# Kernel tuning notes

Measured on AMD Instinct MI355X. Metric: run time of the kernel, lower is better.

Reference implementation:

```python
import jax, jax.numpy as jnp
import numpy as np

NEG = -1e30  # finite stand-in for -inf so logsumexp grads stay finite


def ctc_loss_mean(y_true, log_probs_tm, input_length, label_length, blank=0):
    """CTC loss (forward algorithm in log space), mean over batch.

    log_probs_tm: [T, B, C] time-major log-probabilities.
    y_true:       [B, L] dense int labels (blank=0 excluded from real labels).
    """
    T, B, C = log_probs_tm.shape
    L = y_true.shape[1]
    S = 2 * L + 1  # extended label length: blank, l1, blank, l2, ...
    ll = jnp.clip(label_length, 1, L)
    il = jnp.clip(input_length, 1, T)

    # Extended label sequence: blanks at even positions, labels at odd.
    ext = jnp.full((B, S), blank, dtype=jnp.int32).at[:, 1::2].set(y_true.astype(jnp.int32))
    ext_m2 = jnp.concatenate([jnp.full((B, 2), -1, jnp.int32), ext[:, :-2]], axis=1)
    # Skip transition (s-2 -> s) allowed only for label positions with no repeat.
    allow_skip = ((jnp.arange(S) % 2 == 1)[None, :]) & (ext != ext_m2)

    lp0 = jnp.take_along_axis(log_probs_tm[0], ext, axis=1)  # [B, S]
    alpha0 = jnp.full((B, S), NEG, log_probs_tm.dtype)
    alpha0 = alpha0.at[:, 0].set(lp0[:, 0]).at[:, 1].set(lp0[:, 1])

    def step(alpha, xs):
        lp_t, t = xs
        lpe = jnp.take_along_axis(lp_t, ext, axis=1)  # [B, S]
        a1 = jnp.concatenate([jnp.full((B, 1), NEG, alpha.dtype), alpha[:, :-1]], axis=1)
        a2 = jnp.concatenate([jnp.full((B, 2), NEG, alpha.dtype), alpha[:, :-2]], axis=1)
        a2 = jnp.where(allow_skip, a2, NEG)
        new = jax.nn.logsumexp(jnp.stack([alpha, a1, a2]), axis=0) + lpe
        # Freeze alpha once past each example's input_length.
        return jnp.where((t < il)[:, None], new, alpha), None

    alpha, _ = jax.lax.scan(step, alpha0, (log_probs_tm[1:], jnp.arange(1, T)))

    # Loss = -log(alpha[2*ll-1] + alpha[2*ll]) at the final (frozen) time step.
    idx = jnp.stack([2 * ll - 1, 2 * ll], axis=1)  # [B, 2]
    end_vals = jnp.take_along_axis(alpha, idx, axis=1)
    loss = -jax.nn.logsumexp(end_vals, axis=1)
    return jnp.mean(loss)


def setup_inputs() -> dict:
    key = jax.random.key(0)
    kx, kl, ki, kj = jax.random.split(key, 4)
    B, T, C, L = 64, 1024, 128, 256
    # y_pred are probabilities (module applies log), so softmax random logits.
    y_pred = jax.nn.softmax(jax.random.normal(kx, (B, T, C), jnp.float32), axis=-1)
    y_true = jax.random.randint(kl, (B, L), 1, C, jnp.int32)  # blank=0 excluded
    input_length = jax.random.randint(ki, (B,), T // 2, T + 1, jnp.int32)
    label_length = jax.random.randint(kj, (B,), L // 2, L + 1, jnp.int32)
    return {"y_true": y_true, "y_pred": y_pred,
            "input_length": input_length, "label_length": label_length}


def reference(y_true, y_pred, input_length, label_length):
    # Mirror CTCLayer.call: log + transpose to time-major, reshape lengths.
    log_tm = jnp.log(jnp.transpose(y_pred, (1, 0, 2)))  # [T, B, C]
    loss = ctc_loss_mean(y_true, log_tm,
                         input_length.reshape(-1), label_length.reshape(-1),
                         blank=0)
    return log_tm, loss
```

## Files before the change

### kernel.cpp

```cpp
#include <hip/hip_runtime.h>
#include <math.h>

constexpr int B = 64;
constexpr int T = 1024;
constexpr int C = 128;
constexpr int L = 256;
constexpr int S = 2 * L + 1;
constexpr int TRB = 2048;

template <int N> struct IC { static constexpr int value = N; };

__device__ __forceinline__ float shr1(float x) {
#if __has_builtin(__builtin_amdgcn_mov_dpp)
    return __int_as_float(__builtin_amdgcn_mov_dpp(
        __float_as_int(x), 0x138 , 0xf, 0xf, true));
#else
    return __int_as_float(__builtin_amdgcn_update_dpp(
        0, __float_as_int(x), 0x138, 0xf, 0xf, true));
#endif
}

template <int CTRL>
__device__ __forceinline__ float maxdpp(float x) {
#if __has_builtin(__builtin_amdgcn_mov_dpp)
    float t = __int_as_float(__builtin_amdgcn_mov_dpp(
        __float_as_int(x), CTRL, 0xf, 0xf, true));
#else
    float t = __int_as_float(__builtin_amdgcn_update_dpp(
        0, __float_as_int(x), CTRL, 0xf, 0xf, true));
#endif
    return fmaxf(x, t);
}

__device__ __forceinline__ float wave_max_dpp(float x) {
    x = maxdpp<0x111>(x);
    x = maxdpp<0x112>(x);
    x = maxdpp<0x114>(x);
    x = maxdpp<0x118>(x);
    x = maxdpp<0x142>(x);
    x = maxdpp<0x143>(x);
    return __int_as_float(__builtin_amdgcn_readlane(__float_as_int(x), 63));
}

__global__
__attribute__((amdgpu_waves_per_eu(1, 1)))
__launch_bounds__(64)
void ctc_fused(
    const float* __restrict__ yp,
    const int*   __restrict__ yt,
    const int*   __restrict__ il_,
    const int*   __restrict__ ll_,
    float* __restrict__ out_log,
    float* __restrict__ out_loss)
{
    const int lane = threadIdx.x;
    if (blockIdx.x >= B) {
        int id = blockIdx.x - B;
        int bb = id >> 5;
        int ck = id & 31;
        const float4* src = (const float4*)yp + ((size_t)bb * T + ck * 32) * 32;
        float4* o4 = (float4*)out_log;
        #pragma unroll
        for (int k = 0; k < 16; ++k) {
            int o = k * 64 + lane;
            float4 v = src[o];
            int tt = ck * 32 + (o >> 5);
            int c4 = o & 31;
            float4 r;
            r.x = __logf(v.x); r.y = __logf(v.y);
            r.z = __logf(v.z); r.w = __logf(v.w);
            o4[((size_t)tt * B + bb) * 32 + c4] = r;
        }
        return;
    }

    const int b = blockIdx.x;

    __shared__ float afin[S];

    int il = il_[b]; il = min(max(il, 1), T);
    int ll = ll_[b]; ll = min(max(ll, 1), L);
    const float* yb = yp + (size_t)b * T * C;

    int4 y4 = *(const int4*)(yt + b * L + 4 * lane);
    int  pw = yt[b * L + (lane ? 4 * lane - 1 : 0)];

    float skf4 = (lane && (y4.x != pw))   ? 1.f : 0.f;
    float skf5 = (y4.y != y4.x) ? 1.f : 0.f;
    float skf6 = (y4.z != y4.y) ? 1.f : 0.f;
    float skf7 = (y4.w != y4.z) ? 1.f : 0.f;

    const int c0 = y4.x, c1 = y4.y, c2 = y4.z, c3 = y4.w;

    int z0;
    asm volatile("v_mov_b32 %0, 0" : "=v"(z0));

    float gv[3][4][4], gbv[3][4];

    auto fill = [&](auto Qc, int r0) {
        constexpr int Q = decltype(Qc)::value;
        int r = r0 < T - 4 ? r0 : T - 4;
        const float* rb = yb + (size_t)r * C;
        #pragma unroll
        for (int j = 0; j < 4; ++j) {
            gbv[Q][j]   = rb[j * C + z0];
            gv[Q][j][0] = rb[j * C + c0];
            gv[Q][j][1] = rb[j * C + c1];
            gv[Q][j][2] = rb[j * C + c2];
            gv[Q][j][3] = rb[j * C + c3];
        }
    };

    float p00 = yb[0];
    float p0l = yb[c0];

    fill(IC<0>{}, 1);
    fill(IC<1>{}, 5);

    float a[9];
    #pragma unroll
    for (int i = 0; i < 9; ++i) a[i] = 0.f;
    if (lane == 0) { a[0] = p00; a[1] = p0l; }

    int lsi = 0;
    int t0 = 0;

    auto step = [&](float gb, float g0, float g1, float g2, float g3) {
        float hh = shr1(a[7]);
        float n0 = (a[0] + hh)                      * gb;
        float n1 = fmaf(skf4, hh,   a[1] + a[0])    * g0;
        float n2 = (a[2] + a[1])                    * gb;
        float n3 = fmaf(skf5, a[1], a[3] + a[2])    * g1;
        float n4 = (a[4] + a[3])                    * gb;
        float n5 = fmaf(skf6, a[3], a[5] + a[4])    * g2;
        float n6 = (a[6] + a[5])                    * gb;
        float n7 = fmaf(skf7, a[5], a[7] + a[6])    * g3;
        float n8 = (a[8] + a[7])                    * gb;
        a[0] = n0; a[1] = n1; a[2] = n2; a[3] = n3; a[4] = n4;
        a[5] = n5; a[6] = n6; a[7] = n7; a[8] = n8;
    };

    auto group = [&](auto Pc) {
        constexpr int P = decltype(Pc)::value;
        constexpr int F = (P + 2) % 3;
        #pragma unroll
        for (int j = 0; j < 4; ++j)
            step(gbv[P][j], gv[P][j][0], gv[P][j][1], gv[P][j][2], gv[P][j][3]);
        fill(IC<F>{}, t0 + 9);
        __builtin_amdgcn_sched_barrier(0x7);
        t0 += 4;
    };

    auto maxw = [&]() {
        float m0 = fmaxf(fmaxf(a[0], a[1]), a[2]);
        float m1 = fmaxf(fmaxf(a[3], a[4]), a[5]);
        float m2 = fmaxf(fmaxf(a[6], a[7]), a[8]);
        return fmaxf(fmaxf(m0, m1), m2);
    };

    int pinv_bits = 127 << 23;
    int psh = 0;
    auto measure = [&]() {
        float mm = wave_max_dpp(maxw());
        int eb = (__float_as_int(mm) >> 23) & 0xff;
        int sh = 350 - eb;
        sh = sh > 254 ? 254 : (sh < 1 ? 1 : sh);
        pinv_bits = sh << 23;
        psh = sh - 127;
    };
    auto apply = [&]() {
        float inv = __int_as_float(pinv_bits);
        #pragma unroll
        for (int i = 0; i < 9; ++i) a[i] *= inv;
        lsi -= psh;
    };
    auto rescale = [&]() { measure(); apply(); };

    const int full_end = ((il - 1) >> 2) << 2;

    while (t0 + 24 <= full_end) {
        group(IC<0>{});
        apply();
        group(IC<1>{});
        measure();
        group(IC<2>{});
        apply();
        group(IC<0>{});
        measure();
        group(IC<1>{});
        apply();
        group(IC<2>{});
        measure();
    }
    apply();

    if (t0 + 4 <= full_end) { group(IC<0>{}); rescale(); }
    if (t0 + 4 <= full_end) { group(IC<1>{}); rescale(); }
    if (t0 + 4 <= full_end) { group(IC<2>{}); rescale(); }
    if (t0 + 4 <= full_end) { group(IC<0>{}); rescale(); }
    if (t0 + 4 <= full_end) { group(IC<1>{}); }

    const int ph  = (full_end >> 2) % 3;
    const int tsh = (full_end + 1 > T - 4) ? 1 : 0;
    float tg[3][4], tb[3];
    switch (ph) {
    case 0:
        #pragma unroll
        for (int j = 0; j < 3; ++j) { int s_ = j + tsh; tb[j]=gbv[0][s_]; tg[j][0]=gv[0][s_][0]; tg[j][1]=gv[0][s_][1]; tg[j][2]=gv[0][s_][2]; tg[j][3]=gv[0][s_][3]; }
        break;
    case 1:
        #pragma unroll
        for (int j = 0; j < 3; ++j) { int s_ = j + tsh; tb[j]=gbv[1][s_]; tg[j][0]=gv[1][s_][0]; tg[j][1]=gv[1][s_][1]; tg[j][2]=gv[1][s_][2]; tg[j][3]=gv[1][s_][3]; }
        break;
    default:
        #pragma unroll
        for (int j = 0; j < 3; ++j) { int s_ = j + tsh; tb[j]=gbv[2][s_]; tg[j][0]=gv[2][s_][0]; tg[j][1]=gv[2][s_][1]; tg[j][2]=gv[2][s_][2]; tg[j][3]=gv[2][s_][3]; }
        break;
    }
    #pragma unroll
    for (int j = 0; j < 3; ++j) {
        int r = full_end + 1 + j;
        if (r < il)
            step(tb[j], tg[j][0], tg[j][1], tg[j][2], tg[j][3]);
    }

    #pragma unroll
    for (int k = 0; k < 8; ++k) afin[8 * lane + k] = a[k];
    if (lane == 63) afin[512] = a[8];
    __syncthreads();
    if (lane == 0) {
        float e1 = afin[2 * ll - 1];
        float e2 = afin[2 * ll];
        float sum = fmaxf(e1 + e2, 1e-37f);
        float loss = -(__log2f(sum) + (float)lsi) * 0.6931471805599453f;
        atomicAdd(out_loss, loss * (1.0f / (float)B));
    }
}

extern "C" void kernel_launch(void* const* d_in, const int* in_sizes, int n_in,
                              void* d_out, int out_size, void* d_ws, size_t ws_size,
                              hipStream_t stream) {
    const int*   y_true = (const int*)d_in[0];
    const float* y_pred = (const float*)d_in[1];
    const int*   in_len = (const int*)d_in[2];
    const int*   lb_len = (const int*)d_in[3];

    float* out_log  = (float*)d_out;
    float* out_loss = (float*)d_out + (size_t)T * B * C;

    hipMemsetAsync(out_loss, 0, sizeof(float), stream);
    ctc_fused<<<B + TRB, 64, 0, stream>>>(y_pred, y_true, in_len, lb_len,
                                          out_log, out_loss);
}
```

Before: 171.2 us.

## Hand-issue prefetch loads with explicit vmcnt waits and simplify CTC tail

Replaces the compiler-generated gather loads for the emission rows with an inline-asm block of 20 global_load_dword instructions that use SGPR base plus VGPR offsets. Each group now waits with an explicit s_waitcnt vmcnt(20), so the oldest prefetch is complete while the next one stays in flight, and the prefetch is issued before the four recurrence steps. The intent is tighter control of load latency hiding in the serial alpha recursion. The epilogue switch over register buffers is replaced by simple loops that load rows directly, which adds load latency in the tail, and the hand-counted vmcnt must stay in sync with the number of outstanding loads.

```diff
diff --git a/kernel.cpp b/kernel.cpp
--- a/kernel.cpp
+++ b/kernel.cpp
@@ -40,6 +40,41 @@
     x = maxdpp<0x142>(x);
     x = maxdpp<0x143>(x);
     return __int_as_float(__builtin_amdgcn_readlane(__float_as_int(x), 63));
+}
+
+__device__ __forceinline__ void fill20(float (&gb)[4], float (&g)[4][4],
+                                       int vz, int vc0, int vc1, int vc2,
+                                       int vc3, const float* rb) {
+    asm volatile(
+        "global_load_dword %0, %20, %25 offset:0\n\t"
+        "global_load_dword %1, %21, %25 offset:0\n\t"
+        "global_load_dword %2, %22, %25 offset:0\n\t"
+        "global_load_dword %3, %23, %25 offset:0\n\t"
+        "global_load_dword %4, %24, %25 offset:0\n\t"
+        "global_load_dword %5, %20, %25 offset:512\n\t"
+        "global_load_dword %6, %21, %25 offset:512\n\t"
+        "global_load_dword %7, %22, %25 offset:512\n\t"
+        "global_load_dword %8, %23, %25 offset:512\n\t"
+        "global_load_dword %9, %24, %25 offset:512\n\t"
+        "global_load_dword %10, %20, %25 offset:1024\n\t"
+        "global_load_dword %11, %21, %25 offset:1024\n\t"
+        "global_load_dword %12, %22, %25 offset:1024\n\t"
+        "global_load_dword %13, %23, %25 offset:1024\n\t"
+        "global_load_dword %14, %24, %25 offset:1024\n\t"
+        "global_load_dword %15, %20, %25 offset:1536\n\t"
+        "global_load_dword %16, %21, %25 offset:1536\n\t"
+        "global_load_dword %17, %22, %25 offset:1536\n\t"
+        "global_load_dword %18, %23, %25 offset:1536\n\t"
+        "global_load_dword %19, %24, %25 offset:1536"
+        : "=&v"(gb[0]), "=&v"(g[0][0]), "=&v"(g[0][1]),
+          "=&v"(g[0][2]), "=&v"(g[0][3]),
+          "=&v"(gb[1]), "=&v"(g[1][0]), "=&v"(g[1][1]),
+          "=&v"(g[1][2]), "=&v"(g[1][3]),
+          "=&v"(gb[2]), "=&v"(g[2][0]), "=&v"(g[2][1]),
+          "=&v"(g[2][2]), "=&v"(g[2][3]),
+          "=&v"(gb[3]), "=&v"(g[3][0]), "=&v"(g[3][1]),
+          "=&v"(g[3][2]), "=&v"(g[3][3])
+        : "v"(vz), "v"(vc0), "v"(vc1), "v"(vc2), "v"(vc3), "s"(rb));
 }
 
 __global__
@@ -90,10 +125,15 @@
     float skf6 = (y4.z != y4.y) ? 1.f : 0.f;
     float skf7 = (y4.w != y4.z) ? 1.f : 0.f;
 
-    const int c0 = y4.x, c1 = y4.y, c2 = y4.z, c3 = y4.w;
-
-    int z0;
-    asm volatile("v_mov_b32 %0, 0" : "=v"(z0));
+    int vz  = 0;
+    int vc0 = y4.x * 4, vc1 = y4.y * 4, vc2 = y4.z * 4, vc3 = y4.w * 4;
+
+    float p00 = yb[0];
+    float p0l = yb[y4.x];
+    float a[9];
+    #pragma unroll
+    for (int i = 0; i < 9; ++i) a[i] = 0.f;
+    if (lane == 0) { a[0] = p00; a[1] = p0l; }
 
     float gv[3][4][4], gbv[3][4];
 
@@ -101,26 +141,17 @@
         constexpr int Q = decltype(Qc)::value;
         int r = r0 < T - 4 ? r0 : T - 4;
         const float* rb = yb + (size_t)r * C;
-        #pragma unroll
-        for (int j = 0; j < 4; ++j) {
-            gbv[Q][j]   = rb[j * C + z0];
-            gv[Q][j][0] = rb[j * C + c0];
-            gv[Q][j][1] = rb[j * C + c1];
-            gv[Q][j][2] = rb[j * C + c2];
-            gv[Q][j][3] = rb[j * C + c3];
-        }
-    };
-
-    float p00 = yb[0];
-    float p0l = yb[c0];
-
-    fill(IC<0>{}, 1);
-    fill(IC<1>{}, 5);
-
-    float a[9];
-    #pragma unroll
-    for (int i = 0; i < 9; ++i) a[i] = 0.f;
-    if (lane == 0) { a[0] = p00; a[1] = p0l; }
+        fill20(gbv[Q], gv[Q], vz, vc0, vc1, vc2, vc3, rb);
+    };
+
+    auto wait20 = [&]() {
+        asm volatile("s_waitcnt vmcnt(20)");
+        __builtin_amdgcn_sched_barrier(0);
+    };
+    auto wait0 = [&]() {
+        asm volatile("s_waitcnt vmcnt(0)");
+        __builtin_amdgcn_sched_barrier(0);
+    };
 
     int lsi = 0;
     int t0 = 0;
@@ -140,14 +171,14 @@
         a[5] = n5; a[6] = n6; a[7] = n7; a[8] = n8;
     };
 
-    auto group = [&](auto Pc) {
+    auto groupW = [&](auto Pc) {
         constexpr int P = decltype(Pc)::value;
         constexpr int F = (P + 2) % 3;
+        wait20();
+        fill(IC<F>{}, t0 + 9);
         #pragma unroll
         for (int j = 0; j < 4; ++j)
             step(gbv[P][j], gv[P][j][0], gv[P][j][1], gv[P][j][2], gv[P][j][3]);
-        fill(IC<F>{}, t0 + 9);
-        __builtin_amdgcn_sched_barrier(0x7);
         t0 += 4;
     };
 
@@ -178,50 +209,41 @@
 
     const int full_end = ((il - 1) >> 2) << 2;
 
+    fill(IC<0>{}, 1);
+    fill(IC<1>{}, 5);
+    wait0();
+
     while (t0 + 24 <= full_end) {
-        group(IC<0>{});
-        apply();
-        group(IC<1>{});
-        measure();
-        group(IC<2>{});
-        apply();
-        group(IC<0>{});
-        measure();
-        group(IC<1>{});
-        apply();
-        group(IC<2>{});
-        measure();
+        groupW(IC<0>{}); apply();
+        groupW(IC<1>{}); measure();
+        groupW(IC<2>{}); apply();
+        groupW(IC<0>{}); measure();
+        groupW(IC<1>{}); apply();
+        groupW(IC<2>{}); measure();
+        wait0();
     }
     apply();
 
-    if (t0 + 4 <= full_end) { group(IC<0>{}); rescale(); }
-    if (t0 + 4 <= full_end) { group(IC<1>{}); rescale(); }
-    if (t0 + 4 <= full_end) { group(IC<2>{}); rescale(); }
-    if (t0 + 4 <= full_end) { group(IC<0>{}); rescale(); }
-    if (t0 + 4 <= full_end) { group(IC<1>{}); }
-
-    const int ph  = (full_end >> 2) % 3;
-    const int tsh = (full_end + 1 > T - 4) ? 1 : 0;
-    float tg[3][4], tb[3];
-    switch (ph) {
-    case 0:
-        #pragma unroll
-        for (int j = 0; j < 3; ++j) { int s_ = j + tsh; tb[j]=gbv[0][s_]; tg[j][0]=gv[0][s_][0]; tg[j][1]=gv[0][s_][1]; tg[j][2]=gv[0][s_][2]; tg[j][3]=gv[0][s_][3]; }
-        break;
-    case 1:
-        #pragma unroll
-        for (int j = 0; j < 3; ++j) { int s_ = j + tsh; tb[j]=gbv[1][s_]; tg[j][0]=gv[1][s_][0]; tg[j][1]=gv[1][s_][1]; tg[j][2]=gv[1][s_][2]; tg[j][3]=gv[1][s_][3]; }
-        break;
-    default:
-        #pragma unroll
-        for (int j = 0; j < 3; ++j) { int s_ = j + tsh; tb[j]=gbv[2][s_]; tg[j][0]=gv[2][s_][0]; tg[j][1]=gv[2][s_][1]; tg[j][2]=gv[2][s_][2]; tg[j][3]=gv[2][s_][3]; }
-        break;
-    }
-    #pragma unroll
-    for (int j = 0; j < 3; ++j) {
-        int r = full_end + 1 + j;
-        if (r < il)
-            step(tb[j], tg[j][0], tg[j][1], tg[j][2], tg[j][3]);
+    while (t0 + 4 <= full_end) {
+        const float* rp = yb + (size_t)(t0 + 1) * C;
+        float tb4[4], tg4[4][4];
+        #pragma unroll
+        for (int j = 0; j < 4; ++j) {
+            tb4[j]    = rp[j * C];
+            tg4[j][0] = rp[j * C + y4.x];
+            tg4[j][1] = rp[j * C + y4.y];
+            tg4[j][2] = rp[j * C + y4.z];
+            tg4[j][3] = rp[j * C + y4.w];
+        }
+        #pragma unroll
+        for (int j = 0; j < 4; ++j)
+            step(tb4[j], tg4[j][0], tg4[j][1], tg4[j][2], tg4[j][3]);
+        rescale();
+        t0 += 4;
+    }
+    for (int r = t0 + 1; r < il; ++r) {
+        const float* rp = yb + (size_t)r * C;
+        step(rp[0], rp[y4.x], rp[y4.y], rp[y4.z], rp[y4.w]);
     }
 
     #pragma unroll
```

New measurement: 174.0 us. About the same (+1.6%).

## Split CTC alpha recursion across two waves with LDS halo pipeline

Applied to the files above, without the earlier changes.

Each batch's alpha vector is now split across two wavefronts of 64 lanes. Wave 1 runs a few time-groups behind wave 0 and receives the boundary value through a shared-memory halo ring. Per-group maxima are also exchanged through shared memory, so rescaling is folded into the first step's emission factor with delayed exponent bookkeeping, and the step core is hand-written inline asm. The intent is to halve the per-lane serial work on the latency-bound recursion. In exchange it adds a block barrier per group plus pipeline fill and drain, and the transpose/log blocks are resized to 128 threads.

```diff
diff --git a/kernel.cpp b/kernel.cpp
--- a/kernel.cpp
+++ b/kernel.cpp
@@ -6,7 +6,7 @@
 constexpr int C = 128;
 constexpr int L = 256;
 constexpr int S = 2 * L + 1;
-constexpr int TRB = 2048;
+constexpr int TRB = 1024;
 
 template <int N> struct IC { static constexpr int value = N; };
 
@@ -42,9 +42,30 @@
     return __int_as_float(__builtin_amdgcn_readlane(__float_as_int(x), 63));
 }
 
+__device__ __forceinline__ void core4(float& a0, float& a1, float& a2,
+                                      float& a3, float hh, float k0, float k1,
+                                      float gb, float g0, float g1) {
+    float t0, t1, t2, t3;
+    asm volatile(
+        "v_add_f32 %[t3], %[a3], %[a2]\n\t"
+        "v_add_f32 %[t2], %[a2], %[a1]\n\t"
+        "v_add_f32 %[t1], %[a1], %[a0]\n\t"
+        "v_add_f32 %[t0], %[a0], %[hh]\n\t"
+        "v_fma_f32 %[t3], %[k1], %[a1], %[t3]\n\t"
+        "v_fma_f32 %[t1], %[k0], %[hh], %[t1]\n\t"
+        "v_mul_f32 %[a3], %[t3], %[g1]\n\t"
+        "v_mul_f32 %[a2], %[t2], %[gb]\n\t"
+        "v_mul_f32 %[a0], %[t0], %[gb]\n\t"
+        "v_mul_f32 %[a1], %[t1], %[g0]"
+        : [a0]"+v"(a0), [a1]"+v"(a1), [a2]"+v"(a2), [a3]"+v"(a3),
+          [t0]"=&v"(t0), [t1]"=&v"(t1), [t2]"=&v"(t2), [t3]"=&v"(t3)
+        : [hh]"v"(hh), [k0]"v"(k0), [k1]"v"(k1),
+          [gb]"v"(gb), [g0]"v"(g0), [g1]"v"(g1));
+}
+
 __global__
 __attribute__((amdgpu_waves_per_eu(1, 1)))
-__launch_bounds__(64)
+__launch_bounds__(128)
 void ctc_fused(
     const float* __restrict__ yp,
     const int*   __restrict__ yt,
@@ -53,18 +74,18 @@
     float* __restrict__ out_log,
     float* __restrict__ out_loss)
 {
-    const int lane = threadIdx.x;
+    const int tid = threadIdx.x;
     if (blockIdx.x >= B) {
         int id = blockIdx.x - B;
-        int bb = id >> 5;
-        int ck = id & 31;
-        const float4* src = (const float4*)yp + ((size_t)bb * T + ck * 32) * 32;
+        int bb = id >> 4;
+        int ck = id & 15;
+        const float4* src = (const float4*)yp + ((size_t)bb * T + ck * 64) * 32;
         float4* o4 = (float4*)out_log;
         #pragma unroll
         for (int k = 0; k < 16; ++k) {
-            int o = k * 64 + lane;
+            int o = k * 128 + tid;
             float4 v = src[o];
-            int tt = ck * 32 + (o >> 5);
+            int tt = ck * 64 + (o >> 5);
             int c4 = o & 31;
             float4 r;
             r.x = __logf(v.x); r.y = __logf(v.y);
@@ -74,29 +95,31 @@
         return;
     }
 
-    const int b = blockIdx.x;
+    const int lane = tid & 63;
+    const int w    = tid >> 6;
+    const int b    = blockIdx.x;
 
     __shared__ float afin[S];
+    __shared__ __attribute__((aligned(16))) float halo[36];
+    __shared__ float gmx[256][2];
+
+    if (tid < 36) halo[tid] = 0.f;
+    __syncthreads();
 
     int il = il_[b]; il = min(max(il, 1), T);
     int ll = ll_[b]; ll = min(max(ll, 1), L);
     const float* yb = yp + (size_t)b * T * C;
 
-    int4 y4 = *(const int4*)(yt + b * L + 4 * lane);
-    int  pw = yt[b * L + (lane ? 4 * lane - 1 : 0)];
-
-    float skf4 = (lane && (y4.x != pw))   ? 1.f : 0.f;
-    float skf5 = (y4.y != y4.x) ? 1.f : 0.f;
-    float skf6 = (y4.z != y4.y) ? 1.f : 0.f;
-    float skf7 = (y4.w != y4.z) ? 1.f : 0.f;
-
-    const int c0 = y4.x, c1 = y4.y, c2 = y4.z, c3 = y4.w;
-
-    int z0;
-    asm volatile("v_mov_b32 %0, 0" : "=v"(z0));
-
-    float gv[3][4][4], gbv[3][4];
-
+    const int li = 2 * lane + 128 * w;
+    int2 y2 = *(const int2*)(yt + b * L + li);
+    int yprev = yt[b * L + (li ? li - 1 : 0)];
+    float k0 = (li && (y2.x != yprev)) ? 1.f : 0.f;
+    float k1 = (y2.y != y2.x) ? 1.f : 0.f;
+    const int c0 = y2.x, c1 = y2.y;
+
+    int z0; asm volatile("v_mov_b32 %0, 0" : "=v"(z0));
+
+    float gv[3][4][2], gbv[3][4];
     auto fill = [&](auto Qc, int r0) {
         constexpr int Q = decltype(Qc)::value;
         int r = r0 < T - 4 ? r0 : T - 4;
@@ -106,129 +129,119 @@
             gbv[Q][j]   = rb[j * C + z0];
             gv[Q][j][0] = rb[j * C + c0];
             gv[Q][j][1] = rb[j * C + c1];
-            gv[Q][j][2] = rb[j * C + c2];
-            gv[Q][j][3] = rb[j * C + c3];
         }
     };
 
-    float p00 = yb[0];
-    float p0l = yb[c0];
+    float a0 = 0.f, a1 = 0.f, a2 = 0.f, a3 = 0.f, a4 = 0.f;
+    if (tid == 0) { a0 = yb[0]; a1 = yb[c0]; }
 
     fill(IC<0>{}, 1);
     fill(IC<1>{}, 5);
 
-    float a[9];
-    #pragma unroll
-    for (int i = 0; i < 9; ++i) a[i] = 0.f;
-    if (lane == 0) { a[0] = p00; a[1] = p0l; }
-
     int lsi = 0;
-    int t0 = 0;
-
-    auto step = [&](float gb, float g0, float g1, float g2, float g3) {
-        float hh = shr1(a[7]);
-        float n0 = (a[0] + hh)                      * gb;
-        float n1 = fmaf(skf4, hh,   a[1] + a[0])    * g0;
-        float n2 = (a[2] + a[1])                    * gb;
-        float n3 = fmaf(skf5, a[1], a[3] + a[2])    * g1;
-        float n4 = (a[4] + a[3])                    * gb;
-        float n5 = fmaf(skf6, a[3], a[5] + a[4])    * g2;
-        float n6 = (a[6] + a[5])                    * gb;
-        float n7 = fmaf(skf7, a[5], a[7] + a[6])    * g3;
-        float n8 = (a[8] + a[7])                    * gb;
-        a[0] = n0; a[1] = n1; a[2] = n2; a[3] = n3; a[4] = n4;
-        a[5] = n5; a[6] = n6; a[7] = n7; a[8] = n8;
-    };
-
-    auto group = [&](auto Pc) {
+    int p1 = 0, p2 = 0, p3 = 0;
+    const int  Gf  = (il - 1) >> 2;
+    const int  N   = Gf + 3;
+    const bool isb = (tid == 64);
+
+    auto gbody = [&](auto Pc, int own) {
         constexpr int P = decltype(Pc)::value;
         constexpr int F = (P + 2) % 3;
+        int qi = own - 4;
+        float mm = (qi >= 1) ? fmaxf(gmx[qi][0], gmx[qi][1])
+                             : __int_as_float(223 << 23);
+        int eb = (__float_as_int(mm) >> 23) & 0xff;
+        int pr = 223 - eb;
+        int ps = pr - (p1 + p2 + p3);
+        ps = ps > 127 ? 127 : (ps < -126 ? -126 : ps);
+        float inv = __int_as_float((ps + 127) << 23);
+        p3 = p2; p2 = p1; p1 = ps;
+        lsi -= ps;
+        float fgb = gbv[P][0] * inv, fg0 = gv[P][0][0] * inv,
+              fg1 = gv[P][0][1] * inv;
+        float4 hv = make_float4(0.f, 0.f, 0.f, 0.f);
+        if (w == 1) hv = *(const float4*)&halo[(4 * (own - 1)) & 31];
         #pragma unroll
-        for (int j = 0; j < 4; ++j)
-            step(gbv[P][j], gv[P][j][0], gv[P][j][1], gv[P][j][2], gv[P][j][3]);
-        fill(IC<F>{}, t0 + 9);
+        for (int j = 0; j < 4; ++j) {
+            float gbj = (j == 0) ? fgb : gbv[P][j];
+            float g0j = (j == 0) ? fg0 : gv[P][j][0];
+            float g1j = (j == 0) ? fg1 : gv[P][j][1];
+            float hx  = (j == 0) ? hv.x
+                                 : (j == 1 ? hv.y : (j == 2 ? hv.z : hv.w));
+            float hhv = shr1(a3);
+            float hh  = isb ? hx : hhv;
+            float t4  = a4 + a3;
+            core4(a0, a1, a2, a3, hh, k0, k1, gbj, g0j, g1j);
+            a4 = t4 * gbj;
+            if (w == 0)
+                halo[(lane == 63) ? ((4 * own - 3 + j) & 31) : 33] = a3;
+        }
+        float lm = fmaxf(fmaxf(a0, a1), fmaxf(a2, a3));
+        lm = wave_max_dpp(fmaxf(lm, a4));
+        if (lane == 0) gmx[own][w] = lm;
+        fill(IC<F>{}, 4 * own + 5);
         __builtin_amdgcn_sched_barrier(0x7);
-        t0 += 4;
     };
 
-    auto maxw = [&]() {
-        float m0 = fmaxf(fmaxf(a[0], a[1]), a[2]);
-        float m1 = fmaxf(fmaxf(a[3], a[4]), a[5]);
-        float m2 = fmaxf(fmaxf(a[6], a[7]), a[8]);
-        return fmaxf(fmaxf(m0, m1), m2);
+    auto slot = [&](auto Pc, int k) {
+        bool act = (w == 0) ? (k <= Gf) : (k >= 4);
+        if (act) gbody(Pc, (w == 0) ? k : k - 3);
+        __syncthreads();
     };
 
-    int pinv_bits = 127 << 23;
-    int psh = 0;
-    auto measure = [&]() {
-        float mm = wave_max_dpp(maxw());
-        int eb = (__float_as_int(mm) >> 23) & 0xff;
-        int sh = 350 - eb;
-        sh = sh > 254 ? 254 : (sh < 1 ? 1 : sh);
-        pinv_bits = sh << 23;
-        psh = sh - 127;
-    };
-    auto apply = [&]() {
-        float inv = __int_as_float(pinv_bits);
-        #pragma unroll
-        for (int i = 0; i < 9; ++i) a[i] *= inv;
-        lsi -= psh;
-    };
-    auto rescale = [&]() { measure(); apply(); };
-
-    const int full_end = ((il - 1) >> 2) << 2;
-
-    while (t0 + 24 <= full_end) {
-        group(IC<0>{});
-        apply();
-        group(IC<1>{});
-        measure();
-        group(IC<2>{});
-        apply();
-        group(IC<0>{});
-        measure();
-        group(IC<1>{});
-        apply();
-        group(IC<2>{});
-        measure();
-    }
-    apply();
-
-    if (t0 + 4 <= full_end) { group(IC<0>{}); rescale(); }
-    if (t0 + 4 <= full_end) { group(IC<1>{}); rescale(); }
-    if (t0 + 4 <= full_end) { group(IC<2>{}); rescale(); }
-    if (t0 + 4 <= full_end) { group(IC<0>{}); rescale(); }
-    if (t0 + 4 <= full_end) { group(IC<1>{}); }
-
-    const int ph  = (full_end >> 2) % 3;
-    const int tsh = (full_end + 1 > T - 4) ? 1 : 0;
-    float tg[3][4], tb[3];
-    switch (ph) {
-    case 0:
-        #pragma unroll
-        for (int j = 0; j < 3; ++j) { int s_ = j + tsh; tb[j]=gbv[0][s_]; tg[j][0]=gv[0][s_][0]; tg[j][1]=gv[0][s_][1]; tg[j][2]=gv[0][s_][2]; tg[j][3]=gv[0][s_][3]; }
-        break;
-    case 1:
-        #pragma unroll
-        for (int j = 0; j < 3; ++j) { int s_ = j + tsh; tb[j]=gbv[1][s_]; tg[j][0]=gv[1][s_][0]; tg[j][1]=gv[1][s_][1]; tg[j][2]=gv[1][s_][2]; tg[j][3]=gv[1][s_][3]; }
-        break;
-    default:
-        #pragma unroll
-        for (int j = 0; j < 3; ++j) { int s_ = j + tsh; tb[j]=gbv[2][s_]; tg[j][0]=gv[2][s_][0]; tg[j][1]=gv[2][s_][1]; tg[j][2]=gv[2][s_][2]; tg[j][3]=gv[2][s_][3]; }
-        break;
-    }
+    int k = 1;
+    while (k + 2 <= N) {
+        slot(IC<0>{}, k); slot(IC<1>{}, k + 1); slot(IC<2>{}, k + 2);
+        k += 3;
+    }
+    if (k <= N) { slot(IC<0>{}, k); ++k; }
+    if (k <= N) { slot(IC<1>{}, k); ++k; }
+
     #pragma unroll
     for (int j = 0; j < 3; ++j) {
-        int r = full_end + 1 + j;
-        if (r < il)
-            step(tb[j], tg[j][0], tg[j][1], tg[j][2], tg[j][3]);
-    }
-
-    #pragma unroll
-    for (int k = 0; k < 8; ++k) afin[8 * lane + k] = a[k];
-    if (lane == 63) afin[512] = a[8];
+        int r = 4 * Gf + 1 + j;
+        bool run = (r < il);
+        if (run && w == 0) {
+            const float* rp = yb + (size_t)r * C;
+            float gbj = rp[0], g0j = rp[c0], g1j = rp[c1];
+            float hh = shr1(a3);
+            core4(a0, a1, a2, a3, hh, k0, k1, gbj, g0j, g1j);
+            if (lane == 63) halo[r & 31] = a3;
+        }
+        __syncthreads();
+        if (run && w == 1) {
+            const float* rp = yb + (size_t)r * C;
+            float gbj = rp[0], g0j = rp[c0], g1j = rp[c1];
+            float hvs = halo[(r - 1) & 31];
+            float hhv = shr1(a3);
+            float hh  = (lane == 0) ? hvs : hhv;
+            float t4  = a4 + a3;
+            core4(a0, a1, a2, a3, hh, k0, k1, gbj, g0j, g1j);
+            a4 = t4 * gbj;
+        }
+    }
     __syncthreads();
-    if (lane == 0) {
+
+    for (int q = Gf - 3; q <= Gf; ++q) {
+        if (q >= 1) {
+            float mm = fmaxf(gmx[q][0], gmx[q][1]);
+            int eb = (__float_as_int(mm) >> 23) & 0xff;
+            int pr = 223 - eb;
+            int ps = pr - (p1 + p2 + p3);
+            ps = ps > 127 ? 127 : (ps < -126 ? -126 : ps);
+            float inv = __int_as_float((ps + 127) << 23);
+            p3 = p2; p2 = p1; p1 = ps;
+            lsi -= ps;
+            a0 *= inv; a1 *= inv; a2 *= inv; a3 *= inv; a4 *= inv;
+        }
+    }
+
+    int s0 = 256 * w + 4 * lane;
+    afin[s0 + 0] = a0; afin[s0 + 1] = a1;
+    afin[s0 + 2] = a2; afin[s0 + 3] = a3;
+    if (w == 1 && lane == 63) afin[512] = a4;
+    __syncthreads();
+    if (tid == 0) {
         float e1 = afin[2 * ll - 1];
         float e2 = afin[2 * ll];
         float sum = fmaxf(e1 + e2, 1e-37f);
@@ -249,6 +262,6 @@
     float* out_loss = (float*)d_out + (size_t)T * B * C;
 
     hipMemsetAsync(out_loss, 0, sizeof(float), stream);
-    ctc_fused<<<B + TRB, 64, 0, stream>>>(y_pred, y_true, in_len, lb_len,
-                                          out_log, out_loss);
-}
+    ctc_fused<<<B + TRB, 128, 0, stream>>>(y_pred, y_true, in_len, lb_len,
+                                           out_log, out_loss);
+}
```

Result: slower. 244.2 us (+42.6%).
